# Performance work log

Hardware: AMD Instinct MI355X
Metric: run time of the kernel (lower is better)

The kernel has to match this reference:

```python
import jax, jax.numpy as jnp
import numpy as np

P_X, P_H, P_L, P_VT, P_ET, B = 512, 1024, 4, 512, 256, 512
IN_DIM = P_X + 2 * P_H  # concat([x, prev_time_h, prev_layer_h])


def setup_inputs() -> dict:
    key = jax.random.key(0)
    ks = jax.random.split(key, 10)
    sc_in = 1.0 / np.sqrt(IN_DIM)
    sc_lh = 1.0 / np.sqrt(P_L * P_H)
    return {
        "input_x": jax.random.normal(ks[0], (B, P_X), jnp.float32),
        "h_prev": jax.random.normal(ks[1], (P_L, B, P_H), jnp.float32),
        "c_prev": jax.random.normal(ks[2], (P_L, B, P_H), jnp.float32),
        # stacked gate weights: [L, 4 gates (i,f,o,s), h, in_dim]
        "Wg": jax.random.uniform(ks[3], (P_L, 4, P_H, IN_DIM), jnp.float32, -sc_in, sc_in),
        "bg": jax.random.uniform(ks[4], (P_L, 4, P_H), jnp.float32, -sc_in, sc_in),
        "W_y": jax.random.uniform(ks[5], (P_VT, P_L * P_H), jnp.float32, -sc_lh, sc_lh),
        "b_y": jax.random.uniform(ks[6], (P_VT,), jnp.float32, -sc_lh, sc_lh),
        "W_E": jax.random.uniform(ks[7], (P_ET, P_L * P_H), jnp.float32, -sc_lh, sc_lh),
        "b_E": jax.random.uniform(ks[8], (P_ET,), jnp.float32, -sc_lh, sc_lh),
    }


def _controller(input_x, h_prev, c_prev, Wg, bg):
    prev_layer = jnp.zeros((input_x.shape[0], P_H), input_x.dtype)
    hiddens = []
    for i in range(P_L):  # loop over small fixed layer count
        z = jnp.concatenate([input_x, h_prev[i], prev_layer], axis=-1)  # [B, IN_DIM]
        g = jnp.einsum("bd,ghd->bgh", z, Wg[i]) + bg[i]  # [B, 4, H], one fused GEMM
        i_g = jax.nn.sigmoid(g[:, 0])
        f_g = jax.nn.sigmoid(g[:, 1])
        o_g = jax.nn.sigmoid(g[:, 2])
        s_g = jnp.tanh(g[:, 3])
        c_new = f_g * c_prev[i] + i_g * s_g
        h_new = o_g * jnp.tanh(c_new)
        hiddens.append(h_new)
        prev_layer = h_new
    return jnp.concatenate(hiddens, axis=-1)  # [B, L*H]


def reference(input_x, h_prev, c_prev, Wg, bg, W_y, b_y, W_E, b_E):
    hidden = _controller(input_x, h_prev, c_prev, Wg, bg)
    output = hidden @ W_y.T + b_y      # [B, v_t]
    interface = hidden @ W_E.T + b_E   # [B, E_t]
    return (output, interface)
```

## Files before the change

kernel.cpp:

```cpp
#include <hip/hip_runtime.h>


typedef short    shortx8  __attribute__((ext_vector_type(8)));
typedef float    floatx16 __attribute__((ext_vector_type(16)));

__device__ __forceinline__ unsigned int f2bf1(float x) {
  unsigned int u = __float_as_uint(x);
  return (u + 0x7fffu + ((u >> 16) & 1u)) >> 16;
}
__device__ __forceinline__ unsigned int f2bf2(float lo, float hi) {
  return f2bf1(lo) | (f2bf1(hi) << 16);
}
__device__ __forceinline__ float sigm(float x) { return 1.f / (1.f + __expf(-x)); }
__device__ __forceinline__ float tanh_(float x) { return 1.f - 2.f / (__expf(2.f * x) + 1.f); }

__global__ __launch_bounds__(256) void prep_a0(const float* __restrict__ x,
                                               const float* __restrict__ hp,
                                               unsigned short* __restrict__ A0) {
  const int l   = blockIdx.y;
  const int idx = blockIdx.x * 256 + threadIdx.x;
  const int b   = idx / 192;
  const int kk  = (idx - b * 192) * 8;
  float v[8];
  if (kk < 512) {
    const float* s = x + (size_t)b * 512 + kk;
#pragma unroll
    for (int i = 0; i < 8; ++i) v[i] = s[i];
  } else {
    const float* s = hp + ((size_t)l * 512 + b) * 1024 + (kk - 512);
#pragma unroll
    for (int i = 0; i < 8; ++i) v[i] = s[i];
  }
  uint4 o;
  o.x = f2bf2(v[0], v[1]); o.y = f2bf2(v[2], v[3]);
  o.z = f2bf2(v[4], v[5]); o.w = f2bf2(v[6], v[7]);
  *(uint4*)(A0 + ((size_t)l * 512 + b) * 1536 + kk) = o;
}

__global__ __launch_bounds__(256, 2) void gemm_gates(
    const unsigned short* __restrict__ A0, const float* __restrict__ Wg,
    const float* __restrict__ bg, float* __restrict__ G) {
  __shared__ __align__(16) unsigned short As[2][128 * 64];
  __shared__ __align__(16) unsigned short Bs[2][128 * 64];
  const int tid = threadIdx.x, lane = tid & 63, wave = tid >> 6;
  const int mbase = blockIdx.x * 128;
  const int nbase = blockIdx.y * 128;
  const int l     = blockIdx.z;
  const unsigned short* Ab = A0 + ((size_t)l * 512 + mbase) * 1536;
  const float*          Bb = Wg + (size_t)l * 4096 * 2560 + (size_t)nbase * 2560;
  const int arow = wave * 8 + (lane >> 3);
  const int akg  = lane & 7;

  uint4  apf[4];
  float4 bpf[8];
  auto loadT = [&](int kt) {
    const int kg = kt * 64;
#pragma unroll
    for (int r = 0; r < 4; ++r)
      apf[r] = *(const uint4*)(Ab + (size_t)(arow + r * 32) * 1536 + kg + akg * 8);
#pragma unroll
    for (int j = 0; j < 8; ++j) {
      const int idx = j * 256 + tid;
      bpf[j] = *(const float4*)(Bb + (size_t)(idx >> 4) * 2560 + kg + (idx & 15) * 4);
    }
  };
  auto storeT = [&](int buf) {
#pragma unroll
    for (int r = 0; r < 4; ++r) {
      const int row = arow + r * 32;
      *(uint4*)(&As[buf][row * 64 + ((akg ^ (row & 7)) * 8)]) = apf[r];
    }
#pragma unroll
    for (int j = 0; j < 8; ++j) {
      const int idx = j * 256 + tid;
      const int n = idx >> 4, kc = (idx & 15) * 4;
      uint2 pk;
      pk.x = f2bf2(bpf[j].x, bpf[j].y);
      pk.y = f2bf2(bpf[j].z, bpf[j].w);
      *(uint2*)(&Bs[buf][n * 64 + (((kc >> 3) ^ (n & 7)) * 8) + (kc & 4)]) = pk;
    }
  };

  floatx16 acc[2][2];
#pragma unroll
  for (int a = 0; a < 2; ++a)
#pragma unroll
    for (int b2 = 0; b2 < 2; ++b2)
#pragma unroll
      for (int r = 0; r < 16; ++r) acc[a][b2][r] = 0.f;

  const int wm = (wave >> 1) * 64, wn = (wave & 1) * 64;
  loadT(0);
  storeT(0);
  __syncthreads();
  for (int kt = 0; kt < 24; ++kt) {
    if (kt + 1 < 24) loadT(kt + 1);
    const int cb = kt & 1;
#pragma unroll
    for (int ks = 0; ks < 4; ++ks) {
      const int gb = ks * 2 + (lane >> 5);
      shortx8 af[2], bfv[2];
#pragma unroll
      for (int sm = 0; sm < 2; ++sm) {
        const int row = wm + sm * 32 + (lane & 31);
        af[sm] = *(const shortx8*)(&As[cb][row * 64 + ((gb ^ (row & 7)) * 8)]);
      }
#pragma unroll
      for (int sn = 0; sn < 2; ++sn) {
        const int row = wn + sn * 32 + (lane & 31);
        bfv[sn] = *(const shortx8*)(&Bs[cb][row * 64 + ((gb ^ (row & 7)) * 8)]);
      }
#pragma unroll
      for (int sm = 0; sm < 2; ++sm)
#pragma unroll
        for (int sn = 0; sn < 2; ++sn)
          acc[sm][sn] = __builtin_amdgcn_mfma_f32_32x32x16_bf16(
              af[sm], bfv[sn], acc[sm][sn], 0, 0, 0);
    }
    if (kt + 1 < 24) storeT((kt + 1) & 1);
    __syncthreads();
  }

  const float* bgl = bg + (size_t)l * 4096;
  float* Gl = G + ((size_t)l * 512 + mbase) * 4096;
#pragma unroll
  for (int sm = 0; sm < 2; ++sm)
#pragma unroll
    for (int sn = 0; sn < 2; ++sn) {
      const int col = nbase + wn + sn * 32 + (lane & 31);
      const float bias = bgl[col];
#pragma unroll
      for (int r = 0; r < 16; ++r) {
        const int row = wm + sm * 32 + ((r & 3) + 8 * (r >> 2) + 4 * (lane >> 5));
        Gl[(size_t)row * 4096 + col] = acc[sm][sn][r] + bias;
      }
    }
}

__global__ __launch_bounds__(256) void cell0(const float* __restrict__ G,
                                             const float* __restrict__ cp_l,
                                             unsigned short* __restrict__ hidden) {
  const int idx = (blockIdx.x * 256 + threadIdx.x) * 4;
  const int b = idx >> 10, h = idx & 1023;
  const float* g0 = G + (size_t)b * 4096;
  const float4 vi = *(const float4*)(g0 + h);
  const float4 vf = *(const float4*)(g0 + 1024 + h);
  const float4 vo = *(const float4*)(g0 + 2048 + h);
  const float4 vs = *(const float4*)(g0 + 3072 + h);
  const float4 cp = *(const float4*)(cp_l + (size_t)b * 1024 + h);
  const float gi[4] = {vi.x, vi.y, vi.z, vi.w};
  const float gf[4] = {vf.x, vf.y, vf.z, vf.w};
  const float go[4] = {vo.x, vo.y, vo.z, vo.w};
  const float gs[4] = {vs.x, vs.y, vs.z, vs.w};
  const float cc[4] = {cp.x, cp.y, cp.z, cp.w};
  float hn[4];
#pragma unroll
  for (int j = 0; j < 4; ++j) {
    const float c = sigm(gf[j]) * cc[j] + sigm(gi[j]) * tanh_(gs[j]);
    hn[j] = sigm(go[j]) * tanh_(c);
  }
  uint2 o;
  o.x = f2bf2(hn[0], hn[1]);
  o.y = f2bf2(hn[2], hn[3]);
  *(uint2*)(hidden + (size_t)b * 4096 + h) = o;
}

__global__ __launch_bounds__(512, 2) void gemm_seq_cell(
    const unsigned short* __restrict__ hidden_ro, const float* __restrict__ Wg,
    const float* __restrict__ G, const float* __restrict__ c_prev,
    unsigned short* __restrict__ hidden_w, int l) {
  __shared__ __align__(16) unsigned char raw[49152];
  unsigned short* As = (unsigned short*)raw;
  unsigned short* Bs = (unsigned short*)(raw + 32768);
  float*          Gex = (float*)raw;
  const int tid = threadIdx.x, lane = tid & 63, wave = tid >> 6;
  const int mbase = blockIdx.x * 128;
  const int h0    = blockIdx.y * 16;
  const unsigned short* Ab = hidden_ro + (size_t)(l - 1) * 1024;
  const float*          Bl = Wg + (size_t)l * 4096 * 2560 + 1536;

  uint4  apf[2];
  float4 bpf[2];
  auto loadT = [&](int kt) {
    const int kg = kt * 64;
#pragma unroll
    for (int r = 0; r < 2; ++r) {
      const int row = (tid >> 3) + r * 64;
      apf[r] = *(const uint4*)(Ab + (size_t)(mbase + row) * 4096 + kg + (tid & 7) * 8);
    }
#pragma unroll
    for (int j = 0; j < 2; ++j) {
      const int idx = j * 512 + tid;
      const int nl = idx >> 4, kc = (idx & 15) * 4;
      const int grow = (nl >> 4) * 1024 + h0 + (nl & 15);
      bpf[j] = *(const float4*)(Bl + (size_t)grow * 2560 + kg + kc);
    }
  };
  auto storeT = [&](int buf) {
#pragma unroll
    for (int r = 0; r < 2; ++r) {
      const int row = (tid >> 3) + r * 64;
      *(uint4*)(&As[buf * 8192 + row * 64 + (((tid & 7) ^ (row & 7)) * 8)]) = apf[r];
    }
#pragma unroll
    for (int j = 0; j < 2; ++j) {
      const int idx = j * 512 + tid;
      const int nl = idx >> 4, kc = (idx & 15) * 4;
      uint2 pk;
      pk.x = f2bf2(bpf[j].x, bpf[j].y);
      pk.y = f2bf2(bpf[j].z, bpf[j].w);
      *(uint2*)(&Bs[buf * 4096 + nl * 64 + (((kc >> 3) ^ (nl & 7)) * 8) + (kc & 4)]) = pk;
    }
  };

  floatx16 acc;
#pragma unroll
  for (int r = 0; r < 16; ++r) acc[r] = 0.f;
  const int wm = (wave & 3) * 32, wn = (wave >> 2) * 32;

  loadT(0);
  storeT(0);
  __syncthreads();
  for (int kt = 0; kt < 16; ++kt) {
    if (kt + 1 < 16) loadT(kt + 1);
    const int cb = kt & 1;
    const int rowa = wm + (lane & 31);
    const int rowb = wn + (lane & 31);
#pragma unroll
    for (int ks = 0; ks < 4; ++ks) {
      const int gb = ks * 2 + (lane >> 5);
      const shortx8 af = *(const shortx8*)(&As[cb * 8192 + rowa * 64 + ((gb ^ (rowa & 7)) * 8)]);
      const shortx8 bfv = *(const shortx8*)(&Bs[cb * 4096 + rowb * 64 + ((gb ^ (rowb & 7)) * 8)]);
      acc = __builtin_amdgcn_mfma_f32_32x32x16_bf16(af, bfv, acc, 0, 0, 0);
    }
    if (kt + 1 < 16) storeT((kt + 1) & 1);
    __syncthreads();
  }

  {
    const int col = wn + (lane & 31);
#pragma unroll
    for (int r = 0; r < 16; ++r) {
      const int row = wm + ((r & 3) + 8 * (r >> 2) + 4 * (lane >> 5));
      Gex[row * 65 + col] = acc[r];
    }
  }
  __syncthreads();

  const int hh = tid & 15, q = tid >> 4;
#pragma unroll
  for (int bi = 0; bi < 4; ++bi) {
    const int bl = bi * 32 + q;
    const int b  = mbase + bl;
    const int hg = h0 + hh;
    const float* Gb = G + ((size_t)l * 512 + b) * 4096;
    float gv[4];
#pragma unroll
    for (int g = 0; g < 4; ++g)
      gv[g] = Gex[bl * 65 + g * 16 + hh] + Gb[g * 1024 + hg];
    const float c_old = c_prev[((size_t)l * 512 + b) * 1024 + hg];
    const float c  = sigm(gv[1]) * c_old + sigm(gv[0]) * tanh_(gv[3]);
    const float hn = sigm(gv[2]) * tanh_(c);
    hidden_w[(size_t)b * 4096 + l * 1024 + hg] = (unsigned short)f2bf1(hn);
  }
}

__global__ __launch_bounds__(256) void gemm_heads(
    const unsigned short* __restrict__ A, const float* __restrict__ Wy,
    const float* __restrict__ WE, float* __restrict__ Cp) {
  __shared__ __align__(16) unsigned short As[2][128 * 64];
  __shared__ __align__(16) unsigned short Bs[2][128 * 64];
  const int tid = threadIdx.x, lane = tid & 63, wave = tid >> 6;
  const int mbase = blockIdx.z * 128;
  const int nt    = blockIdx.y;
  const int nbase = nt * 128;
  const float* Bb = (nt < 4) ? (Wy + (size_t)nbase * 4096)
                             : (WE + (size_t)(nbase - 512) * 4096);
  const int k0 = blockIdx.x * 512;
  const unsigned short* Ab = A + (size_t)mbase * 4096;
  const int arow = wave * 8 + (lane >> 3);
  const int akg  = lane & 7;

  uint4  apf[4];
  float4 bpf[8];
  auto loadT = [&](int kt) {
    const int kg = k0 + kt * 64;
#pragma unroll
    for (int r = 0; r < 4; ++r)
      apf[r] = *(const uint4*)(Ab + (size_t)(arow + r * 32) * 4096 + kg + akg * 8);
#pragma unroll
    for (int j = 0; j < 8; ++j) {
      const int idx = j * 256 + tid;
      bpf[j] = *(const float4*)(Bb + (size_t)(idx >> 4) * 4096 + kg + (idx & 15) * 4);
    }
  };
  auto storeT = [&](int buf) {
#pragma unroll
    for (int r = 0; r < 4; ++r) {
      const int row = arow + r * 32;
      *(uint4*)(&As[buf][row * 64 + ((akg ^ (row & 7)) * 8)]) = apf[r];
    }
#pragma unroll
    for (int j = 0; j < 8; ++j) {
      const int idx = j * 256 + tid;
      const int n = idx >> 4, kc = (idx & 15) * 4;
      uint2 pk;
      pk.x = f2bf2(bpf[j].x, bpf[j].y);
      pk.y = f2bf2(bpf[j].z, bpf[j].w);
      *(uint2*)(&Bs[buf][n * 64 + (((kc >> 3) ^ (n & 7)) * 8) + (kc & 4)]) = pk;
    }
  };

  floatx16 acc[2][2];
#pragma unroll
  for (int a = 0; a < 2; ++a)
#pragma unroll
    for (int b2 = 0; b2 < 2; ++b2)
#pragma unroll
      for (int r = 0; r < 16; ++r) acc[a][b2][r] = 0.f;
  const int wm = (wave >> 1) * 64, wn = (wave & 1) * 64;

  loadT(0);
  storeT(0);
  __syncthreads();
  for (int kt = 0; kt < 8; ++kt) {
    if (kt + 1 < 8) loadT(kt + 1);
    const int cb = kt & 1;
#pragma unroll
    for (int ks = 0; ks < 4; ++ks) {
      const int gb = ks * 2 + (lane >> 5);
      shortx8 af[2], bfv[2];
#pragma unroll
      for (int sm = 0; sm < 2; ++sm) {
        const int row = wm + sm * 32 + (lane & 31);
        af[sm] = *(const shortx8*)(&As[cb][row * 64 + ((gb ^ (row & 7)) * 8)]);
      }
#pragma unroll
      for (int sn = 0; sn < 2; ++sn) {
        const int row = wn + sn * 32 + (lane & 31);
        bfv[sn] = *(const shortx8*)(&Bs[cb][row * 64 + ((gb ^ (row & 7)) * 8)]);
      }
#pragma unroll
      for (int sm = 0; sm < 2; ++sm)
#pragma unroll
        for (int sn = 0; sn < 2; ++sn)
          acc[sm][sn] = __builtin_amdgcn_mfma_f32_32x32x16_bf16(
              af[sm], bfv[sn], acc[sm][sn], 0, 0, 0);
    }
    if (kt + 1 < 8) storeT((kt + 1) & 1);
    __syncthreads();
  }

  float* Co = Cp + (size_t)blockIdx.x * 512 * 768;
#pragma unroll
  for (int sm = 0; sm < 2; ++sm)
#pragma unroll
    for (int sn = 0; sn < 2; ++sn) {
      const int col = nbase + wn + sn * 32 + (lane & 31);
#pragma unroll
      for (int r = 0; r < 16; ++r) {
        const int row = mbase + wm + sm * 32 +
                        ((r & 3) + 8 * (r >> 2) + 4 * (lane >> 5));
        Co[(size_t)row * 768 + col] = acc[sm][sn][r];
      }
    }
}

__global__ __launch_bounds__(256) void head_reduce(
    const float* __restrict__ hp, const float* __restrict__ b_y,
    const float* __restrict__ b_E, float* __restrict__ out) {
  const int n = blockIdx.x * 256 + threadIdx.x;
  const int b = blockIdx.y;
  float s = 0.f;
#pragma unroll
  for (int ks = 0; ks < 8; ++ks)
    s += hp[(size_t)ks * 512 * 768 + (size_t)b * 768 + n];
  if (n < 512)
    out[(size_t)b * 512 + n] = s + b_y[n];
  else
    out[(size_t)512 * 512 + (size_t)b * 256 + (n - 512)] = s + b_E[n - 512];
}

extern "C" void kernel_launch(void* const* d_in, const int* in_sizes, int n_in,
                              void* d_out, int out_size, void* d_ws, size_t ws_size,
                              hipStream_t stream) {
  const float* x      = (const float*)d_in[0];
  const float* h_prev = (const float*)d_in[1];
  const float* c_prev = (const float*)d_in[2];
  const float* Wg     = (const float*)d_in[3];
  const float* bg     = (const float*)d_in[4];
  const float* W_y    = (const float*)d_in[5];
  const float* b_y    = (const float*)d_in[6];
  const float* W_E    = (const float*)d_in[7];
  const float* b_E    = (const float*)d_in[8];

  char* ws = (char*)d_ws;
  unsigned short* A0     = (unsigned short*)(ws + 0);
  float*          G      = (float*)(ws + 6291456);
  unsigned short* hidden = (unsigned short*)(ws + 39845888);
  float*          hpart  = (float*)(ws + 44040192);

  prep_a0<<<dim3(384, 4), 256, 0, stream>>>(x, h_prev, A0);
  gemm_gates<<<dim3(4, 32, 4), 256, 0, stream>>>(A0, Wg, bg, G);
  cell0<<<512, 256, 0, stream>>>(G, c_prev, hidden);
  for (int l = 1; l < 4; ++l)
    gemm_seq_cell<<<dim3(4, 64), 512, 0, stream>>>(hidden, Wg, G, c_prev,
                                                   hidden, l);
  gemm_heads<<<dim3(8, 6, 4), 256, 0, stream>>>(hidden, W_y, W_E, hpart);
  head_reduce<<<dim3(3, 512), 256, 0, stream>>>(hpart, b_y, b_E, (float*)d_out);
}
```

Baseline: 404.9 us.

## Deepen GEMM global prefetch to two stages and remap blocks per XCD

All three GEMM kernels now keep two register stages of global prefetch, so tile k+2 is loading while tile k computes. The plain __syncthreads is replaced by an LDS-only waitcnt plus s_barrier, so outstanding global loads are not drained at each barrier. A 1D grid is remapped so that blocks sharing the same weight N-tile land on the same XCD, which is meant to improve L2 reuse of the fp32 weights. The extra prefetch stage costs registers, and gemm_heads also gains a min-occupancy launch bound of 2.

```diff
diff --git a/kernel.cpp b/kernel.cpp
--- a/kernel.cpp
+++ b/kernel.cpp
@@ -13,6 +13,11 @@
 }
 __device__ __forceinline__ float sigm(float x) { return 1.f / (1.f + __expf(-x)); }
 __device__ __forceinline__ float tanh_(float x) { return 1.f - 2.f / (__expf(2.f * x) + 1.f); }
+
+__device__ __forceinline__ void barrier_lgkm() {
+  __builtin_amdgcn_s_waitcnt(0xC07F);
+  __builtin_amdgcn_s_barrier();
+}
 
 __global__ __launch_bounds__(256) void prep_a0(const float* __restrict__ x,
                                                const float* __restrict__ hp,
@@ -40,43 +45,46 @@
 __global__ __launch_bounds__(256, 2) void gemm_gates(
     const unsigned short* __restrict__ A0, const float* __restrict__ Wg,
     const float* __restrict__ bg, float* __restrict__ G) {
-  __shared__ __align__(16) unsigned short As[2][128 * 64];
-  __shared__ __align__(16) unsigned short Bs[2][128 * 64];
+  __shared__ __align__(16) unsigned short As[2][8192];
+  __shared__ __align__(16) unsigned short Bs[2][8192];
   const int tid = threadIdx.x, lane = tid & 63, wave = tid >> 6;
-  const int mbase = blockIdx.x * 128;
-  const int nbase = blockIdx.y * 128;
-  const int l     = blockIdx.z;
+  const int id  = blockIdx.x;
+  const int xcd = id & 7, jj = id >> 3;
+  const int mt  = jj & 3, q = jj >> 2;
+  const int c   = xcd * 16 + q;
+  const int nt  = c & 31, l = c >> 5;
+  const int mbase = mt * 128, nbase = nt * 128;
   const unsigned short* Ab = A0 + ((size_t)l * 512 + mbase) * 1536;
   const float*          Bb = Wg + (size_t)l * 4096 * 2560 + (size_t)nbase * 2560;
   const int arow = wave * 8 + (lane >> 3);
   const int akg  = lane & 7;
 
-  uint4  apf[4];
-  float4 bpf[8];
-  auto loadT = [&](int kt) {
+  uint4  apf[2][4];
+  float4 bpf[2][8];
+  auto loadR = [&](int s, int kt) {
     const int kg = kt * 64;
 #pragma unroll
     for (int r = 0; r < 4; ++r)
-      apf[r] = *(const uint4*)(Ab + (size_t)(arow + r * 32) * 1536 + kg + akg * 8);
-#pragma unroll
-    for (int j = 0; j < 8; ++j) {
-      const int idx = j * 256 + tid;
-      bpf[j] = *(const float4*)(Bb + (size_t)(idx >> 4) * 2560 + kg + (idx & 15) * 4);
-    }
-  };
-  auto storeT = [&](int buf) {
+      apf[s][r] = *(const uint4*)(Ab + (size_t)(arow + r * 32) * 1536 + kg + akg * 8);
+#pragma unroll
+    for (int u = 0; u < 8; ++u) {
+      const int idx = u * 256 + tid;
+      bpf[s][u] = *(const float4*)(Bb + (size_t)(idx >> 4) * 2560 + kg + (idx & 15) * 4);
+    }
+  };
+  auto storeL = [&](int s, int buf) {
 #pragma unroll
     for (int r = 0; r < 4; ++r) {
       const int row = arow + r * 32;
-      *(uint4*)(&As[buf][row * 64 + ((akg ^ (row & 7)) * 8)]) = apf[r];
-    }
-#pragma unroll
-    for (int j = 0; j < 8; ++j) {
-      const int idx = j * 256 + tid;
+      *(uint4*)(&As[buf][row * 64 + ((akg ^ (row & 7)) * 8)]) = apf[s][r];
+    }
+#pragma unroll
+    for (int u = 0; u < 8; ++u) {
+      const int idx = u * 256 + tid;
       const int n = idx >> 4, kc = (idx & 15) * 4;
       uint2 pk;
-      pk.x = f2bf2(bpf[j].x, bpf[j].y);
-      pk.y = f2bf2(bpf[j].z, bpf[j].w);
+      pk.x = f2bf2(bpf[s][u].x, bpf[s][u].y);
+      pk.y = f2bf2(bpf[s][u].z, bpf[s][u].w);
       *(uint2*)(&Bs[buf][n * 64 + (((kc >> 3) ^ (n & 7)) * 8) + (kc & 4)]) = pk;
     }
   };
@@ -88,14 +96,9 @@
     for (int b2 = 0; b2 < 2; ++b2)
 #pragma unroll
       for (int r = 0; r < 16; ++r) acc[a][b2][r] = 0.f;
-
   const int wm = (wave >> 1) * 64, wn = (wave & 1) * 64;
-  loadT(0);
-  storeT(0);
-  __syncthreads();
-  for (int kt = 0; kt < 24; ++kt) {
-    if (kt + 1 < 24) loadT(kt + 1);
-    const int cb = kt & 1;
+
+  auto computeT = [&](int cb) {
 #pragma unroll
     for (int ks = 0; ks < 4; ++ks) {
       const int gb = ks * 2 + (lane >> 5);
@@ -117,8 +120,21 @@
           acc[sm][sn] = __builtin_amdgcn_mfma_f32_32x32x16_bf16(
               af[sm], bfv[sn], acc[sm][sn], 0, 0, 0);
     }
-    if (kt + 1 < 24) storeT((kt + 1) & 1);
-    __syncthreads();
+  };
+
+  loadR(0, 0);
+  loadR(1, 1);
+  storeL(0, 0);
+  barrier_lgkm();
+  for (int kt = 0; kt < 24; kt += 2) {
+    if (kt + 2 < 24) loadR(0, kt + 2);
+    computeT(0);
+    storeL(1, 1);
+    barrier_lgkm();
+    if (kt + 3 < 24) loadR(1, kt + 3);
+    computeT(1);
+    if (kt + 2 < 24) storeL(0, 0);
+    barrier_lgkm();
   }
 
   const float* bgl = bg + (size_t)l * 4096;
@@ -174,41 +190,45 @@
   unsigned short* Bs = (unsigned short*)(raw + 32768);
   float*          Gex = (float*)raw;
   const int tid = threadIdx.x, lane = tid & 63, wave = tid >> 6;
-  const int mbase = blockIdx.x * 128;
-  const int h0    = blockIdx.y * 16;
+  const int id  = blockIdx.x;
+  const int xcd = id & 7, jj = id >> 3;
+  const int mt  = jj & 3, q = jj >> 2;
+  const int ht  = xcd * 8 + q;
+  const int mbase = mt * 128;
+  const int h0    = ht * 16;
   const unsigned short* Ab = hidden_ro + (size_t)(l - 1) * 1024;
   const float*          Bl = Wg + (size_t)l * 4096 * 2560 + 1536;
 
-  uint4  apf[2];
-  float4 bpf[2];
-  auto loadT = [&](int kt) {
+  uint4  apf[2][2];
+  float4 bpf[2][2];
+  auto loadR = [&](int s, int kt) {
     const int kg = kt * 64;
 #pragma unroll
     for (int r = 0; r < 2; ++r) {
       const int row = (tid >> 3) + r * 64;
-      apf[r] = *(const uint4*)(Ab + (size_t)(mbase + row) * 4096 + kg + (tid & 7) * 8);
-    }
-#pragma unroll
-    for (int j = 0; j < 2; ++j) {
-      const int idx = j * 512 + tid;
+      apf[s][r] = *(const uint4*)(Ab + (size_t)(mbase + row) * 4096 + kg + (tid & 7) * 8);
+    }
+#pragma unroll
+    for (int u = 0; u < 2; ++u) {
+      const int idx = u * 512 + tid;
       const int nl = idx >> 4, kc = (idx & 15) * 4;
       const int grow = (nl >> 4) * 1024 + h0 + (nl & 15);
-      bpf[j] = *(const float4*)(Bl + (size_t)grow * 2560 + kg + kc);
-    }
-  };
-  auto storeT = [&](int buf) {
+      bpf[s][u] = *(const float4*)(Bl + (size_t)grow * 2560 + kg + kc);
+    }
+  };
+  auto storeL = [&](int s, int buf) {
 #pragma unroll
     for (int r = 0; r < 2; ++r) {
       const int row = (tid >> 3) + r * 64;
-      *(uint4*)(&As[buf * 8192 + row * 64 + (((tid & 7) ^ (row & 7)) * 8)]) = apf[r];
-    }
-#pragma unroll
-    for (int j = 0; j < 2; ++j) {
-      const int idx = j * 512 + tid;
+      *(uint4*)(&As[buf * 8192 + row * 64 + (((tid & 7) ^ (row & 7)) * 8)]) = apf[s][r];
+    }
+#pragma unroll
+    for (int u = 0; u < 2; ++u) {
+      const int idx = u * 512 + tid;
       const int nl = idx >> 4, kc = (idx & 15) * 4;
       uint2 pk;
-      pk.x = f2bf2(bpf[j].x, bpf[j].y);
-      pk.y = f2bf2(bpf[j].z, bpf[j].w);
+      pk.x = f2bf2(bpf[s][u].x, bpf[s][u].y);
+      pk.y = f2bf2(bpf[s][u].z, bpf[s][u].w);
       *(uint2*)(&Bs[buf * 4096 + nl * 64 + (((kc >> 3) ^ (nl & 7)) * 8) + (kc & 4)]) = pk;
     }
   };
@@ -218,12 +238,7 @@
   for (int r = 0; r < 16; ++r) acc[r] = 0.f;
   const int wm = (wave & 3) * 32, wn = (wave >> 2) * 32;
 
-  loadT(0);
-  storeT(0);
-  __syncthreads();
-  for (int kt = 0; kt < 16; ++kt) {
-    if (kt + 1 < 16) loadT(kt + 1);
-    const int cb = kt & 1;
+  auto computeT = [&](int cb) {
     const int rowa = wm + (lane & 31);
     const int rowb = wn + (lane & 31);
 #pragma unroll
@@ -233,8 +248,21 @@
       const shortx8 bfv = *(const shortx8*)(&Bs[cb * 4096 + rowb * 64 + ((gb ^ (rowb & 7)) * 8)]);
       acc = __builtin_amdgcn_mfma_f32_32x32x16_bf16(af, bfv, acc, 0, 0, 0);
     }
-    if (kt + 1 < 16) storeT((kt + 1) & 1);
-    __syncthreads();
+  };
+
+  loadR(0, 0);
+  loadR(1, 1);
+  storeL(0, 0);
+  barrier_lgkm();
+  for (int kt = 0; kt < 16; kt += 2) {
+    if (kt + 2 < 16) loadR(0, kt + 2);
+    computeT(0);
+    storeL(1, 1);
+    barrier_lgkm();
+    if (kt + 3 < 16) loadR(1, kt + 3);
+    computeT(1);
+    if (kt + 2 < 16) storeL(0, 0);
+    barrier_lgkm();
   }
 
   {
@@ -247,10 +275,10 @@
   }
   __syncthreads();
 
-  const int hh = tid & 15, q = tid >> 4;
+  const int hh = tid & 15, qq = tid >> 4;
 #pragma unroll
   for (int bi = 0; bi < 4; ++bi) {
-    const int bl = bi * 32 + q;
+    const int bl = bi * 32 + qq;
     const int b  = mbase + bl;
     const int hg = h0 + hh;
     const float* Gb = G + ((size_t)l * 512 + b) * 4096;
@@ -265,48 +293,52 @@
   }
 }
 
-__global__ __launch_bounds__(256) void gemm_heads(
+__global__ __launch_bounds__(256, 2) void gemm_heads(
     const unsigned short* __restrict__ A, const float* __restrict__ Wy,
     const float* __restrict__ WE, float* __restrict__ Cp) {
-  __shared__ __align__(16) unsigned short As[2][128 * 64];
-  __shared__ __align__(16) unsigned short Bs[2][128 * 64];
+  __shared__ __align__(16) unsigned short As[2][8192];
+  __shared__ __align__(16) unsigned short Bs[2][8192];
   const int tid = threadIdx.x, lane = tid & 63, wave = tid >> 6;
-  const int mbase = blockIdx.z * 128;
-  const int nt    = blockIdx.y;
+  const int id  = blockIdx.x;
+  const int xcd = id & 7, jj = id >> 3;
+  const int mt  = jj & 3, q = jj >> 2;
+  const int c   = xcd * 6 + q;
+  const int nt  = c % 6, ks0 = c / 6;
+  const int mbase = mt * 128;
   const int nbase = nt * 128;
   const float* Bb = (nt < 4) ? (Wy + (size_t)nbase * 4096)
                              : (WE + (size_t)(nbase - 512) * 4096);
-  const int k0 = blockIdx.x * 512;
+  const int k0 = ks0 * 512;
   const unsigned short* Ab = A + (size_t)mbase * 4096;
   const int arow = wave * 8 + (lane >> 3);
   const int akg  = lane & 7;
 
-  uint4  apf[4];
-  float4 bpf[8];
-  auto loadT = [&](int kt) {
+  uint4  apf[2][4];
+  float4 bpf[2][8];
+  auto loadR = [&](int s, int kt) {
     const int kg = k0 + kt * 64;
 #pragma unroll
     for (int r = 0; r < 4; ++r)
-      apf[r] = *(const uint4*)(Ab + (size_t)(arow + r * 32) * 4096 + kg + akg * 8);
-#pragma unroll
-    for (int j = 0; j < 8; ++j) {
-      const int idx = j * 256 + tid;
-      bpf[j] = *(const float4*)(Bb + (size_t)(idx >> 4) * 4096 + kg + (idx & 15) * 4);
-    }
-  };
-  auto storeT = [&](int buf) {
+      apf[s][r] = *(const uint4*)(Ab + (size_t)(arow + r * 32) * 4096 + kg + akg * 8);
+#pragma unroll
+    for (int u = 0; u < 8; ++u) {
+      const int idx = u * 256 + tid;
+      bpf[s][u] = *(const float4*)(Bb + (size_t)(idx >> 4) * 4096 + kg + (idx & 15) * 4);
+    }
+  };
+  auto storeL = [&](int s, int buf) {
 #pragma unroll
     for (int r = 0; r < 4; ++r) {
       const int row = arow + r * 32;
-      *(uint4*)(&As[buf][row * 64 + ((akg ^ (row & 7)) * 8)]) = apf[r];
-    }
-#pragma unroll
-    for (int j = 0; j < 8; ++j) {
-      const int idx = j * 256 + tid;
+      *(uint4*)(&As[buf][row * 64 + ((akg ^ (row & 7)) * 8)]) = apf[s][r];
+    }
+#pragma unroll
+    for (int u = 0; u < 8; ++u) {
+      const int idx = u * 256 + tid;
       const int n = idx >> 4, kc = (idx & 15) * 4;
       uint2 pk;
-      pk.x = f2bf2(bpf[j].x, bpf[j].y);
-      pk.y = f2bf2(bpf[j].z, bpf[j].w);
+      pk.x = f2bf2(bpf[s][u].x, bpf[s][u].y);
+      pk.y = f2bf2(bpf[s][u].z, bpf[s][u].w);
       *(uint2*)(&Bs[buf][n * 64 + (((kc >> 3) ^ (n & 7)) * 8) + (kc & 4)]) = pk;
     }
   };
@@ -320,12 +352,7 @@
       for (int r = 0; r < 16; ++r) acc[a][b2][r] = 0.f;
   const int wm = (wave >> 1) * 64, wn = (wave & 1) * 64;
 
-  loadT(0);
-  storeT(0);
-  __syncthreads();
-  for (int kt = 0; kt < 8; ++kt) {
-    if (kt + 1 < 8) loadT(kt + 1);
-    const int cb = kt & 1;
+  auto computeT = [&](int cb) {
 #pragma unroll
     for (int ks = 0; ks < 4; ++ks) {
       const int gb = ks * 2 + (lane >> 5);
@@ -347,11 +374,24 @@
           acc[sm][sn] = __builtin_amdgcn_mfma_f32_32x32x16_bf16(
               af[sm], bfv[sn], acc[sm][sn], 0, 0, 0);
     }
-    if (kt + 1 < 8) storeT((kt + 1) & 1);
-    __syncthreads();
-  }
-
-  float* Co = Cp + (size_t)blockIdx.x * 512 * 768;
+  };
+
+  loadR(0, 0);
+  loadR(1, 1);
+  storeL(0, 0);
+  barrier_lgkm();
+  for (int kt = 0; kt < 8; kt += 2) {
+    if (kt + 2 < 8) loadR(0, kt + 2);
+    computeT(0);
+    storeL(1, 1);
+    barrier_lgkm();
+    if (kt + 3 < 8) loadR(1, kt + 3);
+    computeT(1);
+    if (kt + 2 < 8) storeL(0, 0);
+    barrier_lgkm();
+  }
+
+  float* Co = Cp + (size_t)ks0 * 512 * 768;
 #pragma unroll
   for (int sm = 0; sm < 2; ++sm)
 #pragma unroll
@@ -401,11 +441,10 @@
   float*          hpart  = (float*)(ws + 44040192);
 
   prep_a0<<<dim3(384, 4), 256, 0, stream>>>(x, h_prev, A0);
-  gemm_gates<<<dim3(4, 32, 4), 256, 0, stream>>>(A0, Wg, bg, G);
+  gemm_gates<<<512, 256, 0, stream>>>(A0, Wg, bg, G);
   cell0<<<512, 256, 0, stream>>>(G, c_prev, hidden);
   for (int l = 1; l < 4; ++l)
-    gemm_seq_cell<<<dim3(4, 64), 512, 0, stream>>>(hidden, Wg, G, c_prev,
-                                                   hidden, l);
-  gemm_heads<<<dim3(8, 6, 4), 256, 0, stream>>>(hidden, W_y, W_E, hpart);
+    gemm_seq_cell<<<256, 512, 0, stream>>>(hidden, Wg, G, c_prev, hidden, l);
+  gemm_heads<<<192, 256, 0, stream>>>(hidden, W_y, W_E, hpart);
   head_reduce<<<dim3(3, 512), 256, 0, stream>>>(hpart, b_y, b_E, (float*)d_out);
 }
```

New measurement: 462.4 us. 14.2% more time.
